# Performance work log

Measured on AMD Instinct MI355X. Metric: run time of the kernel, lower is better.

## Reference

```python
import jax, jax.numpy as jnp
import numpy as np

T, B, D_IN, E, HA, HB, D_OUT = 64, 64, 4096, 128, 128, 128, 4096


def setup_inputs() -> dict:
    key = jax.random.key(0)
    ks = jax.random.split(key, 18)

    def u(k, shape, fan):
        b = 1.0 / np.sqrt(fan)
        return jax.random.uniform(k, shape, jnp.float32, -b, b)

    return {
        "x": jax.random.uniform(ks[0], (T, B, D_IN), jnp.float32),
        "W_emb": u(ks[1], (E, D_IN), D_IN), "b_emb": u(ks[2], (E,), D_IN),
        "W_ih_a": u(ks[3], (3 * HA, E), HA), "W_hh_a": u(ks[4], (3 * HA, HA), HA),
        "b_ih_a": u(ks[5], (3 * HA,), HA), "b_hh_a": u(ks[6], (3 * HA,), HA),
        "W_ih_b": u(ks[7], (3 * HB, E), HB), "W_hh_b": u(ks[8], (3 * HB, HB), HB),
        "b_ih_b": u(ks[9], (3 * HB,), HB), "b_hh_b": u(ks[10], (3 * HB,), HB),
        "w_alpha": u(ks[11], (1, HA), HA), "b_alpha": u(ks[12], (1,), HA),
        "W_beta": u(ks[13], (E, HB), HB), "b_beta": u(ks[14], (E,), HB),
        "W_out": u(ks[15], (D_OUT, E), E), "b_out": u(ks[16], (D_OUT,), E),
    }


def _gru_states(emb, W_ih, W_hh, b_ih, b_hh):
    # For every query position i, run a GRU over the reversed prefix
    # emb[i], emb[i-1], ..., emb[0] from h0 = 0. All T queries are batched.
    # Returns hs[s, i, b, h] = hidden of query i after step s (input emb[i-s]).
    Tlen, Bsz, _ = emb.shape
    H = W_hh.shape[1]
    i_arr = jnp.arange(Tlen)

    def step(h, s):
        idx = jnp.clip(i_arr - s, 0, Tlen - 1)          # (T,) input index per query
        xs = emb[idx]                                    # (T, B, E)
        gi = xs @ W_ih.T + b_ih                          # (T, B, 3H)
        gh = h @ W_hh.T + b_hh
        i_r, i_z, i_n = jnp.split(gi, 3, axis=-1)
        h_r, h_z, h_n = jnp.split(gh, 3, axis=-1)
        r = jax.nn.sigmoid(i_r + h_r)
        z = jax.nn.sigmoid(i_z + h_z)
        n = jnp.tanh(i_n + r * h_n)
        h_new = (1.0 - z) * n + z * h
        return h_new, h_new

    h0 = jnp.zeros((Tlen, Bsz, H), emb.dtype)
    _, hs = jax.lax.scan(step, h0, jnp.arange(Tlen))
    return hs  # (S, T, B, H)


def _retain_forward(x, W_emb, b_emb, W_ih_a, W_hh_a, b_ih_a, b_hh_a,
                    W_ih_b, W_hh_b, b_ih_b, b_hh_b, w_alpha, b_alpha,
                    W_beta, b_beta, W_out, b_out):
    Tlen = x.shape[0]
    emb = x @ W_emb.T + b_emb                            # (T, B, E)

    hs_a = _gru_states(emb, W_ih_a, W_hh_a, b_ih_a, b_hh_a)  # (S, T, B, HA)
    hs_b = _gru_states(emb, W_ih_b, W_hh_b, b_ih_b, b_hh_b)  # (S, T, B, HB)

    i_arr = jnp.arange(Tlen)
    # reverse_h[i, j] = hidden after processing emb[i..j] (reverse order) = hs[i - j, i]
    rev = jnp.clip(i_arr[:, None] - i_arr[None, :], 0, Tlen - 1)  # (T, T)
    rh_a = hs_a[rev, i_arr[:, None]] * 0.5               # (T, T, B, HA)
    rh_b = hs_b[rev, i_arr[:, None]] * 0.5               # (T, T, B, HB)

    mask = (i_arr[None, :] <= i_arr[:, None])            # (T, T): j <= i valid
    logits = jnp.einsum('ijbh,h->ijb', rh_a, w_alpha[0]) + b_alpha[0]
    logits = jnp.where(mask[:, :, None], logits, -1e9)
    alpha = jax.nn.softmax(logits, axis=1)               # softmax over prefix steps j
    alpha = alpha * mask[:, :, None].astype(alpha.dtype)

    beta = jnp.tanh(rh_b @ W_beta.T + b_beta)            # (T, T, B, E)

    # c[i] = mean_{j<=i} alpha[i,j] * beta[i,j] * emb[j]
    c = jnp.einsum('ijb,ijbe->ibe', alpha, beta * emb[None, :, :, :])
    counts = jnp.arange(1, Tlen + 1, dtype=c.dtype)[:, None, None]
    c = c / counts

    return jax.nn.sigmoid(c @ W_out.T + b_out)           # (T, B, D_OUT)


def reference(x, W_emb, b_emb, W_ih_a, W_hh_a, b_ih_a, b_hh_a,
              W_ih_b, W_hh_b, b_ih_b, b_hh_b, w_alpha, b_alpha,
              W_beta, b_beta, W_out, b_out):
    return _retain_forward(x, W_emb, b_emb, W_ih_a, W_hh_a, b_ih_a, b_hh_a,
                           W_ih_b, W_hh_b, b_ih_b, b_hh_b, w_alpha, b_alpha,
                           W_beta, b_beta, W_out, b_out)
```

## Files before the change

kernel.cpp:

```cpp
#include <hip/hip_runtime.h>
#include <hip/hip_bf16.h>


typedef __attribute__((ext_vector_type(8))) short short8;
typedef __attribute__((ext_vector_type(4))) float f32x4;
typedef _Float16 half8 __attribute__((ext_vector_type(8)));

#define MFMA16(a, b, c) __builtin_amdgcn_mfma_f32_16x16x32_bf16((a), (b), (c), 0, 0, 0)

#define LOG2E 1.4426950408889634f
#define TLOG2E 2.8853900817779268f

__device__ __forceinline__ unsigned pkbf(float a, float b) {
  __hip_bfloat162 t = __float22bfloat162_rn(float2{a, b});
  return *reinterpret_cast<unsigned*>(&t);
}
__device__ __forceinline__ float ex2(float x) { return __builtin_amdgcn_exp2f(x); }
__device__ __forceinline__ float rcpa(float x) { return __builtin_amdgcn_rcpf(x); }
__device__ __forceinline__ float tanh2(float y) {
  float e = ex2(-fmaxf(y, -126.0f));
  return (1.0f - e) * rcpa(1.0f + e);
}

#define OFF_GI3    16777216u
#define OFF_WEMB   27262976u
#define OFF_WOUT   28311552u
#define OFF_WHHA   29360128u
#define OFF_WHHB   29458432u
#define OFF_WIH    29556736u
#define OFF_WBETA  29753344u

__global__ void k_prep(const float* W_emb, const float* W_out,
                       const float* W_hh_a, const float* W_hh_b,
                       const float* W_ih_a, const float* W_ih_b,
                       const float* W_beta,
                       unsigned* wemb, unsigned* wout,
                       unsigned* whha, unsigned* whhb,
                       unsigned* wih, unsigned* wbeta) {
  const unsigned total = 630784u;
  for (unsigned idx = blockIdx.x * 256u + threadIdx.x; idx < total;
       idx += gridDim.x * 256u) {
    unsigned i = idx;
    if (i < 262144u) { float2 v = ((const float2*)W_emb)[i]; wemb[i] = pkbf(v.x, v.y); continue; }
    i -= 262144u;
    if (i < 262144u) { float2 v = ((const float2*)W_out)[i]; wout[i] = pkbf(v.x, v.y); continue; }
    i -= 262144u;
    if (i < 24576u) {
      float2 v = ((const float2*)W_hh_a)[i];
      const float sc = ((i >> 13) == 2u) ? TLOG2E : LOG2E;
      whha[i] = pkbf(sc * v.x, sc * v.y); continue;
    }
    i -= 24576u;
    if (i < 24576u) {
      float2 v = ((const float2*)W_hh_b)[i];
      const float sc = ((i >> 13) == 2u) ? TLOG2E : LOG2E;
      whhb[i] = pkbf(sc * v.x, sc * v.y); continue;
    }
    i -= 24576u;
    if (i < 24576u) {
      float2 v = ((const float2*)W_ih_a)[i];
      const float sc = ((i >> 13) == 2u) ? TLOG2E : LOG2E;
      wih[i] = pkbf(sc * v.x, sc * v.y); continue;
    }
    i -= 24576u;
    if (i < 24576u) {
      float2 v = ((const float2*)W_ih_b)[i];
      const float sc = ((i >> 13) == 2u) ? TLOG2E : LOG2E;
      wih[24576u + i] = pkbf(sc * v.x, sc * v.y); continue;
    }
    i -= 24576u;
    { float2 v = ((const float2*)W_beta)[i]; wbeta[i] = pkbf(LOG2E * v.x, LOG2E * v.y); }
  }
}

__global__ __launch_bounds__(512) void k_front(const float* __restrict__ x,
                                               const unsigned short* __restrict__ wemb,
                                               const unsigned short* __restrict__ wih,
                                               const float* __restrict__ b_emb,
                                               const float* __restrict__ b_ih_a,
                                               const float* __restrict__ b_ih_b,
                                               const float* __restrict__ b_hh_a,
                                               const float* __restrict__ b_hh_b,
                                               _Float16* __restrict__ gih) {
  const int tid = threadIdx.x, w = tid >> 6, lane = tid & 63, q = lane >> 4, ln = lane & 15;
  const int m0 = blockIdx.x * 16;

  __shared__ float part[8][16][132];
  __shared__ unsigned short embs[16][136];

  const f32x4 zero = {0.f, 0.f, 0.f, 0.f};

  {
    f32x4 acc[8];
#pragma unroll
    for (int nt = 0; nt < 8; ++nt) acc[nt] = zero;

    const float* xp = x + (size_t)(m0 + ln) * 4096 + w * 512 + q * 8;
    const unsigned short* wp = wemb + (size_t)ln * 4096 + w * 512 + q * 8;

#pragma unroll 4
    for (int kk = 0; kk < 16; ++kk) {
      const int ko = kk * 32;
      float4 u0 = *(const float4*)(xp + ko);
      float4 u1 = *(const float4*)(xp + ko + 4);
      union { short8 v; unsigned u[4]; } a0;
      a0.u[0] = pkbf(u0.x, u0.y); a0.u[1] = pkbf(u0.z, u0.w);
      a0.u[2] = pkbf(u1.x, u1.y); a0.u[3] = pkbf(u1.z, u1.w);
#pragma unroll
      for (int nt = 0; nt < 8; ++nt) {
        short8 b = *(const short8*)(wp + (size_t)(nt * 16) * 4096 + ko);
        acc[nt] = MFMA16(a0.v, b, acc[nt]);
      }
    }
#pragma unroll
    for (int nt = 0; nt < 8; ++nt)
#pragma unroll
      for (int r = 0; r < 4; ++r)
        part[w][q * 4 + r][nt * 16 + ln] = acc[nt][r];
  }
  __syncthreads();

  {
    const int row = tid & 15, col0 = (tid >> 4) * 4;
    f32x4 s = *(const f32x4*)(b_emb + col0);
#pragma unroll
    for (int ww = 0; ww < 8; ++ww) {
      const f32x4 v = *(const f32x4*)&part[ww][row][col0];
      s[0] += v[0]; s[1] += v[1]; s[2] += v[2]; s[3] += v[3];
    }
    _Float16* g6 = gih + (size_t)(m0 + row) * 1024 + 6;
#pragma unroll
    for (int j = 0; j < 4; ++j) g6[(size_t)(col0 + j) * 8] = (_Float16)s[j];
    *(unsigned*)&embs[row][col0]     = pkbf(s[0], s[1]);
    *(unsigned*)&embs[row][col0 + 2] = pkbf(s[2], s[3]);
  }
  __syncthreads();

  {
    short8 af[4];
#pragma unroll
    for (int kc = 0; kc < 4; ++kc)
      af[kc] = *(const short8*)&embs[ln][kc * 32 + q * 8];

    const int nb = w * 96;
    f32x4 acg[6];
#pragma unroll
    for (int nt = 0; nt < 6; ++nt) acg[nt] = zero;

#pragma unroll
    for (int kc = 0; kc < 4; ++kc) {
      const int ko = kc * 32 + q * 8;
#pragma unroll
      for (int nt = 0; nt < 6; ++nt) {
        short8 b = *(const short8*)(wih + (size_t)(nb + nt * 16 + ln) * 128 + ko);
        acg[nt] = MFMA16(af[kc], b, acg[nt]);
      }
    }
#pragma unroll
    for (int nt = 0; nt < 6; ++nt) {
      const int g = nb + nt * 16 + ln;
      const int gg = g >> 7, kout = g & 127;
      float bias;
      if (g < 384) bias = b_ih_a[g] + ((gg < 2) ? b_hh_a[g] : 0.0f);
      else {
        const int g2 = g - 384;
        bias = b_ih_b[g2] + ((gg < 5) ? b_hh_b[g2] : 0.0f);
      }
      bias *= (gg == 2 || gg == 5) ? TLOG2E : LOG2E;
#pragma unroll
      for (int r = 0; r < 4; ++r)
        gih[(size_t)(m0 + q * 4 + r) * 1024 + kout * 8 + gg] = (_Float16)(acg[nt][r] + bias);
    }
  }
}

__global__ __launch_bounds__(512) __attribute__((amdgpu_waves_per_eu(2, 2)))
void k_recur(const _Float16* __restrict__ gih,
             const unsigned short* __restrict__ whha, const unsigned short* __restrict__ whhb,
             const unsigned short* __restrict__ wbeta,
             const float* __restrict__ b_hh_a, const float* __restrict__ b_hh_b,
             const float* __restrict__ b_beta, const float* __restrict__ b_alpha,
             const float* __restrict__ w_alpha,
             const unsigned short* __restrict__ wout,
             const float* __restrict__ b_out,
             float* __restrict__ out) {
  const int tid = threadIdx.x, w = tid >> 6, lane = tid & 63, q = lane >> 4, ln = lane & 15;
  const int p = blockIdx.x >> 3, btile = blockIdx.x & 7;
  const int i1 = p, i2 = 63 - p;
  const int kout = w * 16 + ln;

  __shared__ unsigned short hA[2][16 * 136], hB[2][16 * 136];

  for (int idx = tid; idx < 16 * 136; idx += 512) { hA[0][idx] = 0; hB[0][idx] = 0; }

  const int iq = (q < 2) ? i1 : i2;
  const _Float16* gp[4];
#pragma unroll
  for (int r = 0; r < 4; ++r) {
    const int b = btile * 8 + (q & 1) * 4 + r;
    gp[r] = gih + (size_t)(iq * 64 + b) * 1024 + kout * 8;
  }

  short8 fra[3][4], frb[3][4];
#pragma unroll
  for (int g = 0; g < 3; ++g) {
    const unsigned short* ba = whha + (size_t)(g * 128 + kout) * 128;
    const unsigned short* bb = whhb + (size_t)(g * 128 + kout) * 128;
#pragma unroll
    for (int kc = 0; kc < 4; ++kc) {
      fra[g][kc] = *(const short8*)(ba + kc * 32 + q * 8);
      frb[g][kc] = *(const short8*)(bb + kc * 32 + q * 8);
    }
  }
#pragma unroll
  for (int g = 0; g < 3; ++g)
#pragma unroll
    for (int kc = 0; kc < 4; ++kc) {
      asm volatile("" : "+a"(fra[g][kc]));
      asm volatile("" : "+a"(frb[g][kc]));
    }

  short8 fbe[4];
#pragma unroll
  for (int kc = 0; kc < 4; ++kc) {
    fbe[kc] = *(const short8*)(wbeta + (size_t)(w * 16 + ln) * 128 + kc * 32 + q * 8);
    asm volatile("" : "+a"(fbe[kc]));
  }

  short8 fal[4];
#pragma unroll
  for (int kc = 0; kc < 4; ++kc) {
    float4 w0 = *(const float4*)(w_alpha + kc * 32 + q * 8);
    float4 w1 = *(const float4*)(w_alpha + kc * 32 + q * 8 + 4);
    union { short8 v; unsigned u[4]; } t;
    t.u[0] = pkbf(0.5f * LOG2E * w0.x, 0.5f * LOG2E * w0.y);
    t.u[1] = pkbf(0.5f * LOG2E * w0.z, 0.5f * LOG2E * w0.w);
    t.u[2] = pkbf(0.5f * LOG2E * w1.x, 0.5f * LOG2E * w1.y);
    t.u[3] = pkbf(0.5f * LOG2E * w1.z, 0.5f * LOG2E * w1.w);
    fal[kc] = t.v;
    asm volatile("" : "+a"(fal[kc]));
  }

  const float bhnA = TLOG2E * b_hh_a[256 + kout];
  const float bhnB = TLOG2E * b_hh_b[256 + kout];
  const float bbet = TLOG2E * b_beta[kout];
  const float bal = LOG2E * b_alpha[0];

  float hRA[4], hRB[4], cac[4], lreg[4], embp[4];
#pragma unroll
  for (int r = 0; r < 4; ++r) { hRA[r] = 0.f; hRB[r] = 0.f; cac[r] = 0.f; lreg[r] = 0.f; embp[r] = 0.f; }

  const f32x4 zero = {0.f, 0.f, 0.f, 0.f};
  int jj = iq;
  half8 ngv[4];
#pragma unroll
  for (int r = 0; r < 4; ++r) ngv[r] = *(const half8*)gp[r];

  __syncthreads();

  for (int s = 0; s <= i2; ++s) {
    const int rb = s & 1, wb = rb ^ 1;

    half8 gv[4];
#pragma unroll
    for (int r = 0; r < 4; ++r) gv[r] = ngv[r];

    short8 haf[4], hbf[4];
#pragma unroll
    for (int kc = 0; kc < 4; ++kc) {
      haf[kc] = *(const short8*)(hA[rb] + ln * 136 + kc * 32 + q * 8);
      hbf[kc] = *(const short8*)(hB[rb] + ln * 136 + kc * 32 + q * 8);
    }

    f32x4 accA[3] = {zero, zero, zero}, accB[3] = {zero, zero, zero};
    f32x4 accV = zero, accL = zero;
#pragma unroll
    for (int kc = 0; kc < 4; ++kc) {
#pragma unroll
      for (int g = 0; g < 3; ++g) {
        accA[g] = MFMA16(haf[kc], fra[g][kc], accA[g]);
        accB[g] = MFMA16(hbf[kc], frb[g][kc], accB[g]);
      }
      accV = MFMA16(hbf[kc], fbe[kc], accV);
      accL = MFMA16(haf[kc], fal[kc], accL);
    }

    const bool act = ((unsigned)(s - 1) <= (unsigned)iq);
#pragma unroll
    for (int r = 0; r < 4; ++r) {
      const float logit = accL[r] + bal;
      const float pp = act ? ex2(logit) : 0.0f;
      lreg[r] += pp;
      const float beta = tanh2(accV[r] + bbet);
      cac[r] += pp * beta * embp[r];
    }

#pragma unroll
    for (int r = 0; r < 4; ++r) {
      const int rowoff = (q * 4 + r) * 136 + kout;

      const float erA = ex2(-((float)gv[r][0] + accA[0][r]));
      const float rA = rcpa(1.0f + erA);
      const float tA = (float)gv[r][2] + rA * (accA[2][r] + bhnA);
      const float enA = ex2(-fmaxf(tA, -62.0f));
      const float ezA = ex2(-fmaxf((float)gv[r][1] + accA[1][r], -62.0f));
      const float apnA = 1.0f + enA, apzA = 1.0f + ezA;
      const float numA = fmaf(hRA[r], apnA, ezA * (1.0f - enA));
      const float hnA = numA * rcpa(apnA * apzA);
      hRA[r] = hnA;
      hA[wb][rowoff] = (unsigned short)pkbf(hnA, hnA);

      const float erB = ex2(-((float)gv[r][3] + accB[0][r]));
      const float rB = rcpa(1.0f + erB);
      const float tB = (float)gv[r][5] + rB * (accB[2][r] + bhnB);
      const float enB = ex2(-fmaxf(tB, -62.0f));
      const float ezB = ex2(-fmaxf((float)gv[r][4] + accB[1][r], -62.0f));
      const float apnB = 1.0f + enB, apzB = 1.0f + ezB;
      const float numB = fmaf(hRB[r], apnB, ezB * (1.0f - enB));
      const float hnB = numB * rcpa(apnB * apzB);
      hRB[r] = hnB;
      hB[wb][rowoff] = (unsigned short)pkbf(hnB, hnB);

      embp[r] = (float)gv[r][6];
    }

    if (jj > 0) {
      --jj;
#pragma unroll
      for (int r = 0; r < 4; ++r) gp[r] -= 65536;
    }
#pragma unroll
    for (int r = 0; r < 4; ++r) ngv[r] = *(const half8*)gp[r];

    asm volatile("s_waitcnt lgkmcnt(0)\n\ts_barrier" ::: "memory");
  }

  {
    const int rb2 = (i2 + 1) & 1;
    short8 haf[4], hbf[4];
#pragma unroll
    for (int kc = 0; kc < 4; ++kc) {
      haf[kc] = *(const short8*)(hA[rb2] + ln * 136 + kc * 32 + q * 8);
      hbf[kc] = *(const short8*)(hB[rb2] + ln * 136 + kc * 32 + q * 8);
    }
    f32x4 accV = zero, accL = zero;
#pragma unroll
    for (int kc = 0; kc < 4; ++kc) {
      accV = MFMA16(hbf[kc], fbe[kc], accV);
      accL = MFMA16(haf[kc], fal[kc], accL);
    }
    const bool act = (iq == i2);
#pragma unroll
    for (int r = 0; r < 4; ++r) {
      const float logit = accL[r] + bal;
      const float pp = act ? ex2(logit) : 0.0f;
      lreg[r] += pp;
      const float beta = tanh2(accV[r] + bbet);
      cac[r] += pp * beta * embp[r];
    }
  }

  __syncthreads();
  {
    const int crow0 = (q >= 2 ? 8 : 0) + (q & 1) * 4;
#pragma unroll
    for (int r = 0; r < 4; ++r) {
      const float val = cac[r] * rcpa(lreg[r] * (float)(iq + 1));
      hA[0][(crow0 + r) * 136 + kout] = (unsigned short)pkbf(val, val);
    }
  }
  __syncthreads();

  {
    short8 cb[4];
#pragma unroll
    for (int kc = 0; kc < 4; ++kc)
      cb[kc] = *(const short8*)(hA[0] + ln * 136 + kc * 32 + q * 8);

    const int m_glob = ((ln >= 8) ? i2 : i1) * 64 + btile * 8 + (ln & 7);
    float* orow = out + (size_t)m_glob * 4096;
    const int nb0 = w * 512;

    for (int nt = 0; nt < 32; ++nt) {
      const int n16 = nb0 + nt * 16;
      f32x4 acc = zero;
#pragma unroll
      for (int kc = 0; kc < 4; ++kc) {
        short8 a = *(const short8*)(wout + (size_t)(n16 + ln) * 128 + kc * 32 + q * 8);
        acc = MFMA16(a, cb[kc], acc);
      }
      const int n0 = n16 + q * 4;
      const float4 bo = *(const float4*)(b_out + n0);
      float4 o;
      o.x = rcpa(1.0f + ex2(-LOG2E * (acc[0] + bo.x)));
      o.y = rcpa(1.0f + ex2(-LOG2E * (acc[1] + bo.y)));
      o.z = rcpa(1.0f + ex2(-LOG2E * (acc[2] + bo.z)));
      o.w = rcpa(1.0f + ex2(-LOG2E * (acc[3] + bo.w)));
      *(float4*)(orow + n0) = o;
    }
  }
}

extern "C" void kernel_launch(void* const* d_in, const int* in_sizes, int n_in,
                              void* d_out, int out_size, void* d_ws, size_t ws_size,
                              hipStream_t stream) {
  const float* x      = (const float*)d_in[0];
  const float* W_emb  = (const float*)d_in[1];
  const float* b_emb  = (const float*)d_in[2];
  const float* W_ih_a = (const float*)d_in[3];
  const float* W_hh_a = (const float*)d_in[4];
  const float* b_ih_a = (const float*)d_in[5];
  const float* b_hh_a = (const float*)d_in[6];
  const float* W_ih_b = (const float*)d_in[7];
  const float* W_hh_b = (const float*)d_in[8];
  const float* b_ih_b = (const float*)d_in[9];
  const float* b_hh_b = (const float*)d_in[10];
  const float* w_alpha = (const float*)d_in[11];
  const float* b_alpha = (const float*)d_in[12];
  const float* W_beta = (const float*)d_in[13];
  const float* b_beta = (const float*)d_in[14];
  const float* W_out  = (const float*)d_in[15];
  const float* b_out  = (const float*)d_in[16];
  float* out = (float*)d_out;

  char* ws = (char*)d_ws;
  _Float16*       gih    = (_Float16*)(ws + OFF_GI3);
  unsigned*       wemb   = (unsigned*)(ws + OFF_WEMB);
  unsigned*       wout   = (unsigned*)(ws + OFF_WOUT);
  unsigned*       whha   = (unsigned*)(ws + OFF_WHHA);
  unsigned*       whhb   = (unsigned*)(ws + OFF_WHHB);
  unsigned*       wih    = (unsigned*)(ws + OFF_WIH);
  unsigned*       wbeta  = (unsigned*)(ws + OFF_WBETA);

  k_prep<<<1024, 256, 0, stream>>>(W_emb, W_out, W_hh_a, W_hh_b, W_ih_a, W_ih_b,
                                   W_beta, wemb, wout, whha, whhb, wih, wbeta);
  k_front<<<256, 512, 0, stream>>>(x, (const unsigned short*)wemb,
                                   (const unsigned short*)wih, b_emb,
                                   b_ih_a, b_ih_b, b_hh_a, b_hh_b, gih);
  k_recur<<<256, 512, 0, stream>>>(gih, (const unsigned short*)whha,
                                   (const unsigned short*)whhb, (const unsigned short*)wbeta,
                                   b_hh_a, b_hh_b, b_beta, b_alpha, w_alpha,
                                   (const unsigned short*)wout, b_out, out);
}
```

Baseline: 326.6 us.

## Stage gate writes in LDS, share reciprocals in GRU, prefetch output weights

The embedding kernel now builds the fp16 gate rows in shared memory (reusing the partial-sum buffer) and writes them to global memory as coalesced 16-byte stores. Before, each thread wrote scattered 2-byte elements. The recurrence merges the A and B GRU reciprocals into one rcp each for the r gate and the final divide, cutting transcendental ops on the serial critical path. Clamping exponents to -30 keeps the combined products from overflowing. The output projection software-pipelines the W_out fragment loads one tile ahead. This costs extra registers and an added barrier, and the combined reciprocals may lose a little precision.

```diff
diff --git a/kernel.cpp b/kernel.cpp
--- a/kernel.cpp
+++ b/kernel.cpp
@@ -120,21 +120,26 @@
   }
   __syncthreads();
 
-  {
-    const int row = tid & 15, col0 = (tid >> 4) * 4;
-    f32x4 s = *(const f32x4*)(b_emb + col0);
+  const int rrow = tid & 15, col0 = (tid >> 4) * 4;
+  f32x4 sred = *(const f32x4*)(b_emb + col0);
+  {
 #pragma unroll
     for (int ww = 0; ww < 8; ++ww) {
-      const f32x4 v = *(const f32x4*)&part[ww][row][col0];
-      s[0] += v[0]; s[1] += v[1]; s[2] += v[2]; s[3] += v[3];
-    }
-    _Float16* g6 = gih + (size_t)(m0 + row) * 1024 + 6;
-#pragma unroll
-    for (int j = 0; j < 4; ++j) g6[(size_t)(col0 + j) * 8] = (_Float16)s[j];
-    *(unsigned*)&embs[row][col0]     = pkbf(s[0], s[1]);
-    *(unsigned*)&embs[row][col0 + 2] = pkbf(s[2], s[3]);
-  }
-  __syncthreads();
+      const f32x4 v = *(const f32x4*)&part[ww][rrow][col0];
+      sred[0] += v[0]; sred[1] += v[1]; sred[2] += v[2]; sred[3] += v[3];
+    }
+    *(unsigned*)&embs[rrow][col0]     = pkbf(sred[0], sred[1]);
+    *(unsigned*)&embs[rrow][col0 + 2] = pkbf(sred[2], sred[3]);
+  }
+  __syncthreads();
+
+  _Float16* stage = (_Float16*)&part[0][0][0];
+
+#pragma unroll
+  for (int j = 0; j < 4; ++j) {
+    stage[rrow * 1032 + (col0 + j) * 8 + 6] = (_Float16)sred[j];
+    stage[rrow * 1032 + (col0 + j) * 8 + 7] = (_Float16)0.0f;
+  }
 
   {
     short8 af[4];
@@ -169,7 +174,18 @@
       bias *= (gg == 2 || gg == 5) ? TLOG2E : LOG2E;
 #pragma unroll
       for (int r = 0; r < 4; ++r)
-        gih[(size_t)(m0 + q * 4 + r) * 1024 + kout * 8 + gg] = (_Float16)(acg[nt][r] + bias);
+        stage[(q * 4 + r) * 1032 + kout * 8 + gg] = (_Float16)(acg[nt][r] + bias);
+    }
+  }
+  __syncthreads();
+
+  {
+    const int row2 = tid >> 5, seg = tid & 31;
+#pragma unroll
+    for (int k = 0; k < 4; ++k) {
+      const int off = (seg + k * 32) * 8;
+      *(short8*)(gih + (size_t)(m0 + row2) * 1024 + off) =
+          *(const short8*)(stage + row2 * 1032 + off);
     }
   }
 }
@@ -299,25 +315,30 @@
     for (int r = 0; r < 4; ++r) {
       const int rowoff = (q * 4 + r) * 136 + kout;
 
-      const float erA = ex2(-((float)gv[r][0] + accA[0][r]));
-      const float rA = rcpa(1.0f + erA);
+      const float erA = ex2(-fmaxf((float)gv[r][0] + accA[0][r], -30.0f));
+      const float erB = ex2(-fmaxf((float)gv[r][3] + accB[0][r], -30.0f));
+      const float dA = 1.0f + erA, dB = 1.0f + erB;
+      const float Rr = rcpa(dA * dB);
+      const float rA = Rr * dB, rB = Rr * dA;
+
       const float tA = (float)gv[r][2] + rA * (accA[2][r] + bhnA);
-      const float enA = ex2(-fmaxf(tA, -62.0f));
-      const float ezA = ex2(-fmaxf((float)gv[r][1] + accA[1][r], -62.0f));
+      const float tB = (float)gv[r][5] + rB * (accB[2][r] + bhnB);
+      const float enA = ex2(-fmaxf(tA, -30.0f));
+      const float enB = ex2(-fmaxf(tB, -30.0f));
+      const float ezA = ex2(-fmaxf((float)gv[r][1] + accA[1][r], -30.0f));
+      const float ezB = ex2(-fmaxf((float)gv[r][4] + accB[1][r], -30.0f));
+
       const float apnA = 1.0f + enA, apzA = 1.0f + ezA;
+      const float apnB = 1.0f + enB, apzB = 1.0f + ezB;
       const float numA = fmaf(hRA[r], apnA, ezA * (1.0f - enA));
-      const float hnA = numA * rcpa(apnA * apzA);
+      const float numB = fmaf(hRB[r], apnB, ezB * (1.0f - enB));
+      const float denA = apnA * apzA, denB = apnB * apzB;
+      const float Rc = rcpa(denA * denB);
+      const float hnA = numA * (denB * Rc);
+      const float hnB = numB * (denA * Rc);
+
       hRA[r] = hnA;
       hA[wb][rowoff] = (unsigned short)pkbf(hnA, hnA);
-
-      const float erB = ex2(-((float)gv[r][3] + accB[0][r]));
-      const float rB = rcpa(1.0f + erB);
-      const float tB = (float)gv[r][5] + rB * (accB[2][r] + bhnB);
-      const float enB = ex2(-fmaxf(tB, -62.0f));
-      const float ezB = ex2(-fmaxf((float)gv[r][4] + accB[1][r], -62.0f));
-      const float apnB = 1.0f + enB, apzB = 1.0f + ezB;
-      const float numB = fmaf(hRB[r], apnB, ezB * (1.0f - enB));
-      const float hnB = numB * rcpa(apnB * apzB);
       hRB[r] = hnB;
       hB[wb][rowoff] = (unsigned short)pkbf(hnB, hnB);
 
@@ -380,16 +401,23 @@
     const int m_glob = ((ln >= 8) ? i2 : i1) * 64 + btile * 8 + (ln & 7);
     float* orow = out + (size_t)m_glob * 4096;
     const int nb0 = w * 512;
+    const unsigned short* wbase = wout + (size_t)(nb0 + ln) * 128 + q * 8;
+
+    short8 acur[4], anxt[4];
+#pragma unroll
+    for (int kc = 0; kc < 4; ++kc) acur[kc] = *(const short8*)(wbase + kc * 32);
 
     for (int nt = 0; nt < 32; ++nt) {
-      const int n16 = nb0 + nt * 16;
+      if (nt < 31) {
+#pragma unroll
+        for (int kc = 0; kc < 4; ++kc)
+          anxt[kc] = *(const short8*)(wbase + (size_t)(nt + 1) * 2048 + kc * 32);
+      }
       f32x4 acc = zero;
 #pragma unroll
-      for (int kc = 0; kc < 4; ++kc) {
-        short8 a = *(const short8*)(wout + (size_t)(n16 + ln) * 128 + kc * 32 + q * 8);
-        acc = MFMA16(a, cb[kc], acc);
-      }
-      const int n0 = n16 + q * 4;
+      for (int kc = 0; kc < 4; ++kc) acc = MFMA16(acur[kc], cb[kc], acc);
+
+      const int n0 = nb0 + nt * 16 + q * 4;
       const float4 bo = *(const float4*)(b_out + n0);
       float4 o;
       o.x = rcpa(1.0f + ex2(-LOG2E * (acc[0] + bo.x)));
@@ -397,6 +425,9 @@
       o.z = rcpa(1.0f + ex2(-LOG2E * (acc[2] + bo.z)));
       o.w = rcpa(1.0f + ex2(-LOG2E * (acc[3] + bo.w)));
       *(float4*)(orow + n0) = o;
+
+#pragma unroll
+      for (int kc = 0; kc < 4; ++kc) acur[kc] = anxt[kc];
     }
   }
 }
```

Measured after the change: 328.4 us. Within noise of the previous version (+0.6%).
